# Performance work log

Hardware: AMD Instinct MI355X
Metric: run time of the kernel (lower is better)

Reference implementation:

```python
import jax, jax.numpy as jnp
import numpy as np
from functools import partial

B, S, H = 1, 2048, 1024
F, E, K = 2048, 8, 2


def setup_inputs() -> dict:
    key = jax.random.key(0)
    ks = jax.random.split(key, 7)
    x = jax.random.normal(ks[0], (B, S, H), dtype=jnp.float32)
    weights = jax.random.uniform(ks[1], (B * S, E), dtype=jnp.float32)
    top_weights = jax.random.uniform(ks[2], (B * S, K), dtype=jnp.float32)
    top_experts = jax.random.randint(ks[3], (B * S, K), 0, E).astype(jnp.int64)
    scale = 0.02  # keep activations in a sane range
    w1 = jax.random.normal(ks[4], (E, F, H), dtype=jnp.float32) * scale
    v1 = jax.random.normal(ks[5], (E, F, H), dtype=jnp.float32) * scale
    w2 = jax.random.normal(ks[6], (E, F, H), dtype=jnp.float32) * scale
    return {"x": x, "weights": weights, "top_weights": top_weights,
            "top_experts": top_experts, "w1": w1, "v1": v1, "w2": w2}


def _moe_forward(x, top_weights, top_experts, w1, v1, w2):
    b, s, h = x.shape
    xf = x.reshape(-1, h)  # [T, H]
    n_exp = w1.shape[0]
    # combine weight per (token, expert): sum over top-k slots routed to e
    onehot = jax.nn.one_hot(top_experts, n_exp, dtype=x.dtype)      # [T, K, E]
    cw = jnp.einsum('tk,tke->et', top_weights, onehot)              # [E, T]

    def body(acc, inputs):
        w1e, v1e, w2e, cwe = inputs  # [F,H], [F,H], [F,H], [T]
        gate = jax.nn.silu(xf @ w1e.T)       # [T, F]
        inter = gate * (xf @ v1e.T)          # GLU
        down = inter @ w2e                   # [T, H]
        return acc + cwe[:, None] * down, None

    out, _ = jax.lax.scan(body, jnp.zeros_like(xf), (w1, v1, w2, cw))
    return out.reshape(b, s, h)


def reference(x, weights, top_weights, top_experts, w1, v1, w2):
    # `weights` (full router probs) is accepted but unused, as in the original.
    return _moe_forward(x, top_weights, top_experts, w1, v1, w2)
```

## Files before the change

### kernel.cpp

```cpp
#include <hip/hip_runtime.h>
#include <hip/hip_bf16.h>


#define T_ 2048
#define H_ 1024
#define F_ 2048
#define E_ 8

#define SCAP 768
#define NSLOT (E_ * SCAP)
#define MAXT2 (NSLOT / 128)

typedef unsigned short u16;
typedef short s8v __attribute__((ext_vector_type(8)));
typedef float f4v __attribute__((ext_vector_type(4)));
typedef unsigned short u16x4 __attribute__((ext_vector_type(4)));

__device__ __forceinline__ u16 f2bf(float f) {
    union { float f; unsigned u; } v; v.f = f;
    unsigned r = v.u + 0x7FFF + ((v.u >> 16) & 1);
    return (u16)(r >> 16);
}
__device__ __forceinline__ unsigned pkbf(float a, float b) {
    __hip_bfloat162 h = __float22bfloat162_rn(make_float2(a, b));
    union { __hip_bfloat162 h; unsigned u; } c; c.h = h; return c.u;
}
__device__ __forceinline__ int4 cvt8(const float4 a, const float4 b) {
    int4 r; r.x = (int)pkbf(a.x, a.y); r.y = (int)pkbf(a.z, a.w);
    r.z = (int)pkbf(b.x, b.y); r.w = (int)pkbf(b.z, b.w); return r;
}
__device__ __forceinline__ void async16(void* lds, const void* g) {
    __builtin_amdgcn_global_load_lds(
        (const __attribute__((address_space(1))) unsigned*)g,
        (__attribute__((address_space(3))) unsigned*)lds, 16, 0, 0);
}

__global__ void router_kernel(const int* __restrict__ te, const float* __restrict__ tw,
                              int* __restrict__ slot_tok, float* __restrict__ slot_w,
                              int* __restrict__ tok_slot,
                              int* __restrict__ tile_e, int* __restrict__ tile_s,
                              int* __restrict__ ntiles) {
    __shared__ int cnt[E_];
    __shared__ int s_any;
    int tid = threadIdx.x;
    if (tid < E_) cnt[tid] = 0;
    if (tid == 0) s_any = 0;
    __syncthreads();
    int any = 0;
    for (int i = tid; i < 2 * T_; i += 256) if (i & 1) any |= te[i];
    if (any) atomicOr(&s_any, 1);
    __syncthreads();
    bool is32 = (s_any != 0);
    for (int t = tid; t < T_; t += 256) {
        int e0 = is32 ? te[2 * t]     : te[4 * t];
        int e1 = is32 ? te[2 * t + 1] : te[4 * t + 2];
        float w0 = tw[2 * t], w1 = tw[2 * t + 1];
        if (e0 == e1) {
            int p = atomicAdd(&cnt[e0], 1);
            int s = (p < SCAP) ? e0 * SCAP + p : -1;
            if (s >= 0) { slot_tok[s] = t; slot_w[s] = w0 + w1; }
            tok_slot[2 * t] = s; tok_slot[2 * t + 1] = -1;
        } else {
            int p = atomicAdd(&cnt[e0], 1);
            int s = (p < SCAP) ? e0 * SCAP + p : -1;
            if (s >= 0) { slot_tok[s] = t; slot_w[s] = w0; }
            tok_slot[2 * t] = s;
            p = atomicAdd(&cnt[e1], 1);
            s = (p < SCAP) ? e1 * SCAP + p : -1;
            if (s >= 0) { slot_tok[s] = t; slot_w[s] = w1; }
            tok_slot[2 * t + 1] = s;
        }
    }
    __syncthreads();
    for (int e = 0; e < E_; ++e) {
        int c = min(cnt[e], SCAP);
        int pc = min((c + 127) & ~127, SCAP);
        for (int p = c + tid; p < pc; p += 256) {
            slot_tok[e * SCAP + p] = -1; slot_w[e * SCAP + p] = 0.f;
        }
    }
    __syncthreads();
    if (tid == 0) {
        int nt = 0;
        for (int e = 0; e < E_; ++e) {
            int pc = min((min(cnt[e], SCAP) + 127) & ~127, SCAP);
            for (int s = 0; s < pc; s += 128) { tile_e[nt] = e; tile_s[nt] = e * SCAP + s; ++nt; }
        }
        *ntiles = nt;
    }
}

__global__ void cvtwv_kernel(const float* __restrict__ w1, const float* __restrict__ v1,
                             u16* __restrict__ w1b, u16* __restrict__ v1b) {
    const float* src = blockIdx.y ? v1 : w1;
    u16* dst = blockIdx.y ? v1b : w1b;
    int i = (blockIdx.x * 256 + threadIdx.x) * 4;
    float4 v = *(const float4*)(src + i);
    u16x4 o = { f2bf(v.x), f2bf(v.y), f2bf(v.z), f2bf(v.w) };
    *(u16x4*)(dst + i) = o;
}

__global__ void tcvt8_kernel(const float* __restrict__ src0, u16* __restrict__ dst0) {
    const float* src = src0 + (size_t)blockIdx.z * F_ * H_;
    u16* dst = dst0 + (size_t)blockIdx.z * H_ * F_;
    __shared__ __align__(16) u16 tile[64][72];
    int bc = blockIdx.x * 64, br = blockIdx.y * 64;
    int tx = threadIdx.x, ty = threadIdx.y;
    for (int r = ty; r < 64; r += 32) {
        const float* p = src + (size_t)(br + r) * H_ + bc + tx * 8;
        float4 v0 = *(const float4*)p;
        float4 v1 = *(const float4*)(p + 4);
        u16* q = &tile[r][tx * 8];
        q[0] = f2bf(v0.x); q[1] = f2bf(v0.y); q[2] = f2bf(v0.z); q[3] = f2bf(v0.w);
        q[4] = f2bf(v1.x); q[5] = f2bf(v1.y); q[6] = f2bf(v1.z); q[7] = f2bf(v1.w);
    }
    __syncthreads();
    for (int c = ty; c < 64; c += 32) {
        u16 tmp[8];
#pragma unroll
        for (int j = 0; j < 8; ++j) tmp[j] = tile[tx * 8 + j][c];
        *(int4*)&dst[(size_t)(bc + c) * F_ + br + tx * 8] = *(int4*)tmp;
    }
}

__global__ void gather_x_kernel(const float* __restrict__ x, const int* __restrict__ slot_tok,
                                const int* __restrict__ tile_s, const int* __restrict__ ntiles,
                                u16* __restrict__ xg) {
    if ((int)blockIdx.x >= *ntiles) return;
    int base = tile_s[blockIdx.x];
    int tid = threadIdx.x;
    __shared__ int stok[128];
    if (tid < 128) stok[tid] = slot_tok[base + tid];
    __syncthreads();
    for (int c = tid; c < 128 * 128; c += 256) {
        int r = c >> 7, co = (c & 127) * 8;
        int tok = stok[r];
        u16* dst = xg + ((size_t)(base + r) << 10) + co;
        if (tok < 0) { *(int4*)dst = make_int4(0, 0, 0, 0); }
        else {
            const float* p = x + ((size_t)tok << 10) + co;
            *(int4*)dst = cvt8(*(const float4*)p, *(const float4*)(p + 4));
        }
    }
}

__global__ __launch_bounds__(256, 4) void glu_async_kernel(
        const u16* __restrict__ xg, const u16* __restrict__ w1b,
        const u16* __restrict__ v1b, const int* __restrict__ tile_e,
        const int* __restrict__ tile_s, const int* __restrict__ ntiles,
        const float* __restrict__ slot_w, u16* __restrict__ inter) {
    int bt = blockIdx.y;
    if (bt >= *ntiles) return;
    int e = tile_e[bt], s0 = tile_s[bt];
    int f0 = blockIdx.x * 64;
    __shared__ __align__(16) u16 As[128 * 32];
    __shared__ __align__(16) u16 B1s[64 * 32];
    __shared__ __align__(16) u16 B2s[64 * 32];
    __shared__ float swv[128];
    int tid = threadIdx.x;
    int lane = tid & 63, wave = tid >> 6;
    int wm = wave >> 1, wn = wave & 1;
    int ml = lane & 15, q = lane >> 4;
    if (tid < 128) swv[tid] = slot_w[s0 + tid];

    int acol = (lane & 3) << 3;
    int row0 = (wave << 4) + (lane >> 2);
    int row1 = row0 + 64;
    const u16* gA0  = xg + ((size_t)(s0 + row0) << 10) + acol;
    const u16* gA1  = xg + ((size_t)(s0 + row1) << 10) + acol;
    const size_t wofs = (size_t)e * F_ * H_;
    const u16* gB1 = w1b + wofs + ((size_t)(f0 + row0) << 10) + acol;
    const u16* gB2 = v1b + wofs + ((size_t)(f0 + row0) << 10) + acol;
    u16* lA0 = As  + (row0 << 5) + acol;
    u16* lA1 = As  + (row1 << 5) + acol;
    u16* lB1 = B1s + (row0 << 5) + acol;
    u16* lB2 = B2s + (row0 << 5) + acol;

    f4v accg[4][2] = {};
    f4v accu[4][2] = {};

    for (int k0 = 0; k0 < H_; k0 += 32) {
        __syncthreads();
        async16(lA0, gA0 + k0);
        async16(lA1, gA1 + k0);
        async16(lB1, gB1 + k0);
        async16(lB2, gB2 + k0);
        __syncthreads();
        s8v a[4], b1[2], b2[2];
#pragma unroll
        for (int i = 0; i < 4; ++i)
            a[i]  = *(const s8v*)(As  + (wm * 64 + i * 16 + ml) * 32 + q * 8);
#pragma unroll
        for (int j = 0; j < 2; ++j) {
            b1[j] = *(const s8v*)(B1s + (wn * 32 + j * 16 + ml) * 32 + q * 8);
            b2[j] = *(const s8v*)(B2s + (wn * 32 + j * 16 + ml) * 32 + q * 8);
        }
#pragma unroll
        for (int i = 0; i < 4; ++i)
#pragma unroll
            for (int j = 0; j < 2; ++j) {
                accg[i][j] = __builtin_amdgcn_mfma_f32_16x16x32_bf16(a[i], b1[j], accg[i][j], 0, 0, 0);
                accu[i][j] = __builtin_amdgcn_mfma_f32_16x16x32_bf16(a[i], b2[j], accu[i][j], 0, 0, 0);
            }
    }
#pragma unroll
    for (int i = 0; i < 4; ++i)
#pragma unroll
        for (int r = 0; r < 4; ++r) {
            int lr = wm * 64 + i * 16 + q * 4 + r;
            float cv = swv[lr];
#pragma unroll
            for (int j = 0; j < 2; ++j) {
                float g = accg[i][j][r];
                float u = accu[i][j][r];
                float s = g / (1.f + __expf(-g));
                int f = f0 + wn * 32 + j * 16 + ml;
                inter[((size_t)(s0 + lr) << 11) + f] = f2bf(cv * s * u);
            }
        }
}

__global__ __launch_bounds__(256, 4) void down_async_kernel(
        const u16* __restrict__ inter, const u16* __restrict__ w2bT,
        const int* __restrict__ tile_e, const int* __restrict__ tile_s,
        const int* __restrict__ ntiles,
        float* __restrict__ dbufA, float* __restrict__ dbufB) {
    int bt = blockIdx.y;
    if (bt >= *ntiles) return;
    int e = tile_e[bt], s0 = tile_s[bt];
    int h0 = blockIdx.x * 64;
    int ks = blockIdx.z;
    int kbeg = ks * (F_ / 2);
    float* dbuf = ks ? dbufB : dbufA;
    __shared__ __align__(16) u16 As[128 * 32];
    __shared__ __align__(16) u16 Bs[64 * 32];
    int tid = threadIdx.x;
    int lane = tid & 63, wave = tid >> 6;
    int wm = wave >> 1, wn = wave & 1;
    int ml = lane & 15, q = lane >> 4;

    int acol = (lane & 3) << 3;
    int row0 = (wave << 4) + (lane >> 2);
    int row1 = row0 + 64;
    const u16* gA0 = inter + ((size_t)(s0 + row0) << 11) + kbeg + acol;
    const u16* gA1 = inter + ((size_t)(s0 + row1) << 11) + kbeg + acol;
    const u16* gB  = w2bT + (size_t)e * H_ * F_ + ((size_t)(h0 + row0) << 11) + kbeg + acol;
    u16* lA0 = As + (row0 << 5) + acol;
    u16* lA1 = As + (row1 << 5) + acol;
    u16* lB  = Bs + (row0 << 5) + acol;

    f4v acc[4][2] = {};
    for (int k0 = 0; k0 < F_ / 2; k0 += 32) {
        __syncthreads();
        async16(lA0, gA0 + k0);
        async16(lA1, gA1 + k0);
        async16(lB,  gB  + k0);
        __syncthreads();
        s8v a[4], b[2];
#pragma unroll
        for (int i = 0; i < 4; ++i)
            a[i] = *(const s8v*)(As + (wm * 64 + i * 16 + ml) * 32 + q * 8);
#pragma unroll
        for (int j = 0; j < 2; ++j)
            b[j] = *(const s8v*)(Bs + (wn * 32 + j * 16 + ml) * 32 + q * 8);
#pragma unroll
        for (int i = 0; i < 4; ++i)
#pragma unroll
            for (int j = 0; j < 2; ++j)
                acc[i][j] = __builtin_amdgcn_mfma_f32_16x16x32_bf16(a[i], b[j], acc[i][j], 0, 0, 0);
    }
#pragma unroll
    for (int i = 0; i < 4; ++i)
#pragma unroll
        for (int r = 0; r < 4; ++r) {
            int lr = wm * 64 + i * 16 + q * 4 + r;
            float* drow = dbuf + ((size_t)(s0 + lr) << 10);
#pragma unroll
            for (int j = 0; j < 2; ++j) {
                int h = h0 + wn * 32 + j * 16 + ml;
                drow[h] = acc[i][j][r];
            }
        }
}

__global__ void combine_kernel(const float* __restrict__ dbufA, const float* __restrict__ dbufB,
                               const int* __restrict__ tok_slot, float* __restrict__ out) {
    int t = blockIdx.x;
    int c = threadIdx.x * 4;
    int s0 = tok_slot[2 * t], s1 = tok_slot[2 * t + 1];
    float4 acc = make_float4(0.f, 0.f, 0.f, 0.f);
    if (s0 >= 0) {
        float4 a = *(const float4*)(dbufA + ((size_t)s0 << 10) + c);
        float4 b = *(const float4*)(dbufB + ((size_t)s0 << 10) + c);
        acc.x = a.x + b.x; acc.y = a.y + b.y; acc.z = a.z + b.z; acc.w = a.w + b.w;
    }
    if (s1 >= 0) {
        float4 a = *(const float4*)(dbufA + ((size_t)s1 << 10) + c);
        float4 b = *(const float4*)(dbufB + ((size_t)s1 << 10) + c);
        acc.x += a.x + b.x; acc.y += a.y + b.y; acc.z += a.z + b.z; acc.w += a.w + b.w;
    }
    *(float4*)(out + ((size_t)t << 10) + c) = acc;
}

#define SCAP3 1024
__global__ void router3_kernel(const int* __restrict__ te, const float* __restrict__ tw,
                               int* __restrict__ cnt_g, int* __restrict__ slot_tok,
                               float* __restrict__ slot_w) {
    __shared__ int cnt[E_];
    __shared__ int s_any;
    int tid = threadIdx.x;
    if (tid < E_) cnt[tid] = 0;
    if (tid == 0) s_any = 0;
    __syncthreads();
    int any = 0;
    for (int i = tid; i < 2 * T_; i += 256) if (i & 1) any |= te[i];
    if (any) atomicOr(&s_any, 1);
    __syncthreads();
    bool is32 = (s_any != 0);
    for (int t = tid; t < T_; t += 256) {
        int e0 = is32 ? te[2 * t]     : te[4 * t];
        int e1 = is32 ? te[2 * t + 1] : te[4 * t + 2];
        float w0 = tw[2 * t], w1 = tw[2 * t + 1];
        if (e0 == e1) {
            int p = atomicAdd(&cnt[e0], 1);
            if (p < SCAP3) { slot_tok[e0 * SCAP3 + p] = t; slot_w[e0 * SCAP3 + p] = w0 + w1; }
        } else {
            int p = atomicAdd(&cnt[e0], 1);
            if (p < SCAP3) { slot_tok[e0 * SCAP3 + p] = t; slot_w[e0 * SCAP3 + p] = w0; }
            p = atomicAdd(&cnt[e1], 1);
            if (p < SCAP3) { slot_tok[e1 * SCAP3 + p] = t; slot_w[e1 * SCAP3 + p] = w1; }
        }
    }
    __syncthreads();
    for (int e = 0; e < E_; ++e) {
        int c = min(cnt[e], SCAP3);
        int pc = min((c + 127) & ~127, SCAP3);
        for (int p = c + tid; p < pc; p += 256) {
            slot_tok[e * SCAP3 + p] = 0; slot_w[e * SCAP3 + p] = 0.f;
        }
    }
    if (tid < E_) cnt_g[tid] = min(cnt[tid], SCAP3);
}
__global__ void cvt_kernel(const float* __restrict__ src, u16* __restrict__ dst) {
    int i = (blockIdx.x * 256 + threadIdx.x) * 4;
    float4 v = *(const float4*)(src + i);
    u16x4 o = { f2bf(v.x), f2bf(v.y), f2bf(v.z), f2bf(v.w) };
    *(u16x4*)(dst + i) = o;
}
__global__ __launch_bounds__(256, 2) void glu3_kernel(
        const u16* __restrict__ xb, const float* __restrict__ w1,
        const float* __restrict__ v1, const int* __restrict__ cnt_g,
        const int* __restrict__ slot_tok, const float* __restrict__ slot_w,
        u16* __restrict__ inter) {
    int e = blockIdx.x >> 3, tt = blockIdx.x & 7;
    if (tt * 128 >= cnt_g[e]) return;
    __shared__ __align__(16) u16 As[128 * 32];
    __shared__ __align__(16) u16 B1s[128 * 32];
    __shared__ __align__(16) u16 B2s[128 * 32];
    __shared__ int stok[128];
    __shared__ float sw[128];
    int tid = threadIdx.x;
    if (tid < 128) {
        stok[tid] = slot_tok[e * SCAP3 + tt * 128 + tid];
        sw[tid]   = slot_w[e * SCAP3 + tt * 128 + tid];
    }
    __syncthreads();
    int lane = tid & 63, wave = tid >> 6;
    int wm = wave >> 1, wn = wave & 1;
    int f0 = blockIdx.y * 128;
    int ml = lane & 15, q = lane >> 4;
    int r0 = tid >> 2, r1 = 64 + (tid >> 2);
    int colo = (tid & 3) * 8;
    const size_t tokoff0 = (size_t)stok[r0] * H_ + colo;
    const size_t tokoff1 = (size_t)stok[r1] * H_ + colo;
    const float* gb1 = w1 + (size_t)e * F_ * H_ + (size_t)f0 * H_;
    const float* gb2 = v1 + (size_t)e * F_ * H_ + (size_t)f0 * H_;
    const size_t boff0 = (size_t)r0 * H_ + colo;
    const size_t boff1 = (size_t)r1 * H_ + colo;
    f4v accg[4][4] = {};
    f4v accu[4][4] = {};
    for (int k0 = 0; k0 < H_; k0 += 32) {
        __syncthreads();
        *(int4*)(As + tid * 8)         = *(const int4*)(xb + tokoff0 + k0);
        *(int4*)(As + (256 + tid) * 8) = *(const int4*)(xb + tokoff1 + k0);
        const float* p = gb1 + boff0 + k0;
        *(int4*)(B1s + tid * 8) = cvt8(*(const float4*)p, *(const float4*)(p + 4));
        p = gb1 + boff1 + k0;
        *(int4*)(B1s + (256 + tid) * 8) = cvt8(*(const float4*)p, *(const float4*)(p + 4));
        p = gb2 + boff0 + k0;
        *(int4*)(B2s + tid * 8) = cvt8(*(const float4*)p, *(const float4*)(p + 4));
        p = gb2 + boff1 + k0;
        *(int4*)(B2s + (256 + tid) * 8) = cvt8(*(const float4*)p, *(const float4*)(p + 4));
        __syncthreads();
        s8v a[4], b1[4], b2[4];
#pragma unroll
        for (int i = 0; i < 4; ++i) {
            a[i]  = *(const s8v*)(As  + (wm * 64 + i * 16 + ml) * 32 + q * 8);
            b1[i] = *(const s8v*)(B1s + (wn * 64 + i * 16 + ml) * 32 + q * 8);
            b2[i] = *(const s8v*)(B2s + (wn * 64 + i * 16 + ml) * 32 + q * 8);
        }
#pragma unroll
        for (int i = 0; i < 4; ++i)
#pragma unroll
            for (int j = 0; j < 4; ++j) {
                accg[i][j] = __builtin_amdgcn_mfma_f32_16x16x32_bf16(a[i], b1[j], accg[i][j], 0, 0, 0);
                accu[i][j] = __builtin_amdgcn_mfma_f32_16x16x32_bf16(a[i], b2[j], accu[i][j], 0, 0, 0);
            }
    }
#pragma unroll
    for (int i = 0; i < 4; ++i)
#pragma unroll
        for (int r = 0; r < 4; ++r) {
            int lr = wm * 64 + i * 16 + q * 4 + r;
            float cv = sw[lr];
#pragma unroll
            for (int j = 0; j < 4; ++j) {
                float g = accg[i][j][r];
                float u = accu[i][j][r];
                float s = g / (1.f + __expf(-g));
                int f = f0 + wn * 64 + j * 16 + ml;
                inter[(size_t)(e * SCAP3 + tt * 128 + lr) * F_ + f] = f2bf(cv * s * u);
            }
        }
}
__global__ __launch_bounds__(256) void down3_kernel(
        const u16* __restrict__ inter, const u16* __restrict__ w2bT,
        const int* __restrict__ cnt_g, const int* __restrict__ slot_tok,
        float* __restrict__ out) {
    int e = blockIdx.x >> 3, tt = blockIdx.x & 7;
    if (tt * 128 >= cnt_g[e]) return;
    __shared__ __align__(16) u16 As[128 * 32];
    __shared__ __align__(16) u16 Bs[128 * 32];
    __shared__ int stok[128];
    int tid = threadIdx.x;
    if (tid < 128) stok[tid] = slot_tok[e * SCAP3 + tt * 128 + tid];
    __syncthreads();
    int lane = tid & 63, wave = tid >> 6;
    int wm = wave >> 1, wn = wave & 1;
    int h0 = blockIdx.y * 128;
    int ml = lane & 15, q = lane >> 4;
    int kbeg = blockIdx.z * (F_ / 2), kend = kbeg + (F_ / 2);
    f4v acc[4][4] = {};
    const u16* ga = inter + (size_t)(e * SCAP3 + tt * 128) * F_;
    const u16* gb = w2bT + (size_t)e * H_ * F_ + (size_t)h0 * F_;
    for (int k0 = kbeg; k0 < kend; k0 += 32) {
        __syncthreads();
#pragma unroll
        for (int p = 0; p < 2; ++p) {
            int c = p * 256 + tid;
            int r = c >> 2, co = (c & 3) * 8;
            *(int4*)(As + c * 8) = *(const int4*)(ga + (size_t)r * F_ + k0 + co);
            *(int4*)(Bs + c * 8) = *(const int4*)(gb + (size_t)r * F_ + k0 + co);
        }
        __syncthreads();
        s8v a[4], b[4];
#pragma unroll
        for (int i = 0; i < 4; ++i) {
            a[i] = *(const s8v*)(As + (wm * 64 + i * 16 + ml) * 32 + q * 8);
            b[i] = *(const s8v*)(Bs + (wn * 64 + i * 16 + ml) * 32 + q * 8);
        }
#pragma unroll
        for (int i = 0; i < 4; ++i)
#pragma unroll
            for (int j = 0; j < 4; ++j)
                acc[i][j] = __builtin_amdgcn_mfma_f32_16x16x32_bf16(a[i], b[j], acc[i][j], 0, 0, 0);
    }
#pragma unroll
    for (int i = 0; i < 4; ++i)
#pragma unroll
        for (int r = 0; r < 4; ++r) {
            int lr = wm * 64 + i * 16 + q * 4 + r;
            size_t trow = (size_t)stok[lr] * H_;
#pragma unroll
            for (int j = 0; j < 4; ++j) {
                int h = h0 + wn * 64 + j * 16 + ml;
                atomicAdd(&out[trow + h], acc[i][j][r]);
            }
        }
}

extern "C" void kernel_launch(void* const* d_in, const int* in_sizes, int n_in,
                              void* d_out, int out_size, void* d_ws, size_t ws_size,
                              hipStream_t stream) {
    const float* x  = (const float*)d_in[0];
    const float* tw = (const float*)d_in[2];
    const int*   te = (const int*)d_in[3];
    const float* w1 = (const float*)d_in[4];
    const float* v1 = (const float*)d_in[5];
    const float* w2 = (const float*)d_in[6];
    float* out = (float*)d_out;
    char* ws = (char*)d_ws;

    if (ws_size >= ((size_t)135 << 20)) {
        int*   ntiles   = (int*)(ws);
        int*   tile_e   = (int*)(ws + 256);
        int*   tile_s   = (int*)(ws + 512);
        int*   tok_slot = (int*)(ws + (4 << 10));
        int*   slot_tok = (int*)(ws + (20 << 10));
        float* slot_w   = (float*)(ws + (44 << 10));
        u16*   xg       = (u16*)(ws + ((size_t)1 << 20));
        u16*   w1b      = (u16*)(ws + ((size_t)13 << 20));
        u16*   v1b      = (u16*)(ws + ((size_t)45 << 20));
        u16*   w2bT     = (u16*)(ws + ((size_t)77 << 20));
        u16*   inter    = (u16*)(ws + ((size_t)109 << 20));
        float* dbufA    = (float*)(ws + ((size_t)13 << 20));
        float* dbufB    = (float*)(ws + ((size_t)45 << 20));

        router_kernel<<<1, 256, 0, stream>>>(te, tw, slot_tok, slot_w, tok_slot,
                                             tile_e, tile_s, ntiles);
        cvtwv_kernel<<<dim3((E_ * F_ * H_) / 1024, 2), 256, 0, stream>>>(w1, v1, w1b, v1b);
        tcvt8_kernel<<<dim3(H_ / 64, F_ / 64, E_), dim3(8, 32), 0, stream>>>(w2, w2bT);
        gather_x_kernel<<<MAXT2, 256, 0, stream>>>(x, slot_tok, tile_s, ntiles, xg);
        glu_async_kernel<<<dim3(F_ / 64, MAXT2), 256, 0, stream>>>(
            xg, w1b, v1b, tile_e, tile_s, ntiles, slot_w, inter);
        down_async_kernel<<<dim3(H_ / 64, MAXT2, 2), 256, 0, stream>>>(
            inter, w2bT, tile_e, tile_s, ntiles, dbufA, dbufB);
        combine_kernel<<<T_, 256, 0, stream>>>(dbufA, dbufB, tok_slot, out);
    } else {
        int*   cnt_g    = (int*)(ws);
        int*   slot_tok = (int*)(ws + (4 << 10));
        float* slot_w   = (float*)(ws + (64 << 10));
        u16*   xb       = (u16*)(ws + ((size_t)1 << 20));
        u16*   w2bT     = (u16*)(ws + ((size_t)5 << 20));
        u16*   inter    = (u16*)(ws + ((size_t)37 << 20));

        hipMemsetAsync(out, 0, (size_t)T_ * H_ * sizeof(float), stream);
        router3_kernel<<<1, 256, 0, stream>>>(te, tw, cnt_g, slot_tok, slot_w);
        cvt_kernel<<<(T_ * H_) / 1024, 256, 0, stream>>>(x, xb);
        tcvt8_kernel<<<dim3(H_ / 64, F_ / 64, E_), dim3(8, 32), 0, stream>>>(w2, w2bT);
        glu3_kernel<<<dim3(E_ * 8, F_ / 128), 256, 0, stream>>>(
            xb, w1, v1, cnt_g, slot_tok, slot_w, inter);
        down3_kernel<<<dim3(E_ * 8, H_ / 128, 2), 256, 0, stream>>>(
            inter, w2bT, cnt_g, slot_tok, out);
    }
}
```

Before: 366.1 us.

## Double-buffer LDS with XOR swizzle in GEMMs, widen conversion and gather grids

Both GEMM kernels now double-buffer their LDS tiles. The next k-slice is prefetched with async loads while the current one feeds MFMA, and one barrier per iteration is removed. Column chunks are XOR-swizzled on store and read to cut LDS bank conflicts. The weight conversion kernel handles 8 elements per thread, and the gather kernel is split over 8 y-blocks for more parallelism. The doubled LDS footprint may limit occupancy, and relying on a single barrier assumes the async loads have completed before that barrier.

```diff
diff --git a/kernel.cpp b/kernel.cpp
--- a/kernel.cpp
+++ b/kernel.cpp
@@ -94,10 +94,10 @@
                              u16* __restrict__ w1b, u16* __restrict__ v1b) {
     const float* src = blockIdx.y ? v1 : w1;
     u16* dst = blockIdx.y ? v1b : w1b;
-    int i = (blockIdx.x * 256 + threadIdx.x) * 4;
-    float4 v = *(const float4*)(src + i);
-    u16x4 o = { f2bf(v.x), f2bf(v.y), f2bf(v.z), f2bf(v.w) };
-    *(u16x4*)(dst + i) = o;
+    int i = (blockIdx.x * 256 + threadIdx.x) * 8;
+    float4 a = *(const float4*)(src + i);
+    float4 b = *(const float4*)(src + i + 4);
+    *(int4*)(dst + i) = cvt8(a, b);
 }
 
 __global__ void tcvt8_kernel(const float* __restrict__ src0, u16* __restrict__ dst0) {
@@ -132,7 +132,8 @@
     __shared__ int stok[128];
     if (tid < 128) stok[tid] = slot_tok[base + tid];
     __syncthreads();
-    for (int c = tid; c < 128 * 128; c += 256) {
+    int c0 = blockIdx.y * 2048;
+    for (int c = c0 + tid; c < c0 + 2048; c += 256) {
         int r = c >> 7, co = (c & 127) * 8;
         int tok = stok[r];
         u16* dst = xg + ((size_t)(base + r) << 10) + co;
@@ -153,9 +154,9 @@
     if (bt >= *ntiles) return;
     int e = tile_e[bt], s0 = tile_s[bt];
     int f0 = blockIdx.x * 64;
-    __shared__ __align__(16) u16 As[128 * 32];
-    __shared__ __align__(16) u16 B1s[64 * 32];
-    __shared__ __align__(16) u16 B2s[64 * 32];
+    __shared__ __align__(16) u16 As[2][128 * 32];
+    __shared__ __align__(16) u16 B1s[2][64 * 32];
+    __shared__ __align__(16) u16 B2s[2][64 * 32];
     __shared__ float swv[128];
     int tid = threadIdx.x;
     int lane = tid & 63, wave = tid >> 6;
@@ -163,37 +164,44 @@
     int ml = lane & 15, q = lane >> 4;
     if (tid < 128) swv[tid] = slot_w[s0 + tid];
 
-    int acol = (lane & 3) << 3;
     int row0 = (wave << 4) + (lane >> 2);
     int row1 = row0 + 64;
-    const u16* gA0  = xg + ((size_t)(s0 + row0) << 10) + acol;
-    const u16* gA1  = xg + ((size_t)(s0 + row1) << 10) + acol;
+    int cs = ((lane & 3) ^ ((row0 >> 1) & 3)) << 3;
+    const u16* gA0  = xg + ((size_t)(s0 + row0) << 10) + cs;
+    const u16* gA1  = xg + ((size_t)(s0 + row1) << 10) + cs;
     const size_t wofs = (size_t)e * F_ * H_;
-    const u16* gB1 = w1b + wofs + ((size_t)(f0 + row0) << 10) + acol;
-    const u16* gB2 = v1b + wofs + ((size_t)(f0 + row0) << 10) + acol;
-    u16* lA0 = As  + (row0 << 5) + acol;
-    u16* lA1 = As  + (row1 << 5) + acol;
-    u16* lB1 = B1s + (row0 << 5) + acol;
-    u16* lB2 = B2s + (row0 << 5) + acol;
+    const u16* gB1 = w1b + wofs + ((size_t)(f0 + row0) << 10) + cs;
+    const u16* gB2 = v1b + wofs + ((size_t)(f0 + row0) << 10) + cs;
+    int l0 = (row0 << 5) + ((lane & 3) << 3);
+    int l1 = (row1 << 5) + ((lane & 3) << 3);
+    int xs = (q ^ ((lane >> 1) & 3)) << 3;
 
     f4v accg[4][2] = {};
     f4v accu[4][2] = {};
 
+    async16(&As[0][l0],  gA0);
+    async16(&As[0][l1],  gA1);
+    async16(&B1s[0][l0], gB1);
+    async16(&B2s[0][l0], gB2);
+
+    int cur = 0;
     for (int k0 = 0; k0 < H_; k0 += 32) {
         __syncthreads();
-        async16(lA0, gA0 + k0);
-        async16(lA1, gA1 + k0);
-        async16(lB1, gB1 + k0);
-        async16(lB2, gB2 + k0);
-        __syncthreads();
+        if (k0 + 32 < H_) {
+            int nx = cur ^ 1;
+            async16(&As[nx][l0],  gA0 + k0 + 32);
+            async16(&As[nx][l1],  gA1 + k0 + 32);
+            async16(&B1s[nx][l0], gB1 + k0 + 32);
+            async16(&B2s[nx][l0], gB2 + k0 + 32);
+        }
         s8v a[4], b1[2], b2[2];
 #pragma unroll
         for (int i = 0; i < 4; ++i)
-            a[i]  = *(const s8v*)(As  + (wm * 64 + i * 16 + ml) * 32 + q * 8);
+            a[i]  = *(const s8v*)(&As[cur][(wm * 64 + i * 16 + ml) * 32 + xs]);
 #pragma unroll
         for (int j = 0; j < 2; ++j) {
-            b1[j] = *(const s8v*)(B1s + (wn * 32 + j * 16 + ml) * 32 + q * 8);
-            b2[j] = *(const s8v*)(B2s + (wn * 32 + j * 16 + ml) * 32 + q * 8);
+            b1[j] = *(const s8v*)(&B1s[cur][(wn * 32 + j * 16 + ml) * 32 + xs]);
+            b2[j] = *(const s8v*)(&B2s[cur][(wn * 32 + j * 16 + ml) * 32 + xs]);
         }
 #pragma unroll
         for (int i = 0; i < 4; ++i)
@@ -202,6 +210,7 @@
                 accg[i][j] = __builtin_amdgcn_mfma_f32_16x16x32_bf16(a[i], b1[j], accg[i][j], 0, 0, 0);
                 accu[i][j] = __builtin_amdgcn_mfma_f32_16x16x32_bf16(a[i], b2[j], accu[i][j], 0, 0, 0);
             }
+        cur ^= 1;
     }
 #pragma unroll
     for (int i = 0; i < 4; ++i)
@@ -232,42 +241,51 @@
     int ks = blockIdx.z;
     int kbeg = ks * (F_ / 2);
     float* dbuf = ks ? dbufB : dbufA;
-    __shared__ __align__(16) u16 As[128 * 32];
-    __shared__ __align__(16) u16 Bs[64 * 32];
+    __shared__ __align__(16) u16 As[2][128 * 32];
+    __shared__ __align__(16) u16 Bs[2][64 * 32];
     int tid = threadIdx.x;
     int lane = tid & 63, wave = tid >> 6;
     int wm = wave >> 1, wn = wave & 1;
     int ml = lane & 15, q = lane >> 4;
 
-    int acol = (lane & 3) << 3;
     int row0 = (wave << 4) + (lane >> 2);
     int row1 = row0 + 64;
-    const u16* gA0 = inter + ((size_t)(s0 + row0) << 11) + kbeg + acol;
-    const u16* gA1 = inter + ((size_t)(s0 + row1) << 11) + kbeg + acol;
-    const u16* gB  = w2bT + (size_t)e * H_ * F_ + ((size_t)(h0 + row0) << 11) + kbeg + acol;
-    u16* lA0 = As + (row0 << 5) + acol;
-    u16* lA1 = As + (row1 << 5) + acol;
-    u16* lB  = Bs + (row0 << 5) + acol;
+    int cs = ((lane & 3) ^ ((row0 >> 1) & 3)) << 3;
+    const u16* gA0 = inter + ((size_t)(s0 + row0) << 11) + kbeg + cs;
+    const u16* gA1 = inter + ((size_t)(s0 + row1) << 11) + kbeg + cs;
+    const u16* gB  = w2bT + (size_t)e * H_ * F_ + ((size_t)(h0 + row0) << 11) + kbeg + cs;
+    int l0 = (row0 << 5) + ((lane & 3) << 3);
+    int l1 = (row1 << 5) + ((lane & 3) << 3);
+    int xs = (q ^ ((lane >> 1) & 3)) << 3;
 
     f4v acc[4][2] = {};
+
+    async16(&As[0][l0], gA0);
+    async16(&As[0][l1], gA1);
+    async16(&Bs[0][l0], gB);
+
+    int cur = 0;
     for (int k0 = 0; k0 < F_ / 2; k0 += 32) {
         __syncthreads();
-        async16(lA0, gA0 + k0);
-        async16(lA1, gA1 + k0);
-        async16(lB,  gB  + k0);
-        __syncthreads();
+        if (k0 + 32 < F_ / 2) {
+            int nx = cur ^ 1;
+            async16(&As[nx][l0], gA0 + k0 + 32);
+            async16(&As[nx][l1], gA1 + k0 + 32);
+            async16(&Bs[nx][l0], gB  + k0 + 32);
+        }
         s8v a[4], b[2];
 #pragma unroll
         for (int i = 0; i < 4; ++i)
-            a[i] = *(const s8v*)(As + (wm * 64 + i * 16 + ml) * 32 + q * 8);
+            a[i] = *(const s8v*)(&As[cur][(wm * 64 + i * 16 + ml) * 32 + xs]);
 #pragma unroll
         for (int j = 0; j < 2; ++j)
-            b[j] = *(const s8v*)(Bs + (wn * 32 + j * 16 + ml) * 32 + q * 8);
+            b[j] = *(const s8v*)(&Bs[cur][(wn * 32 + j * 16 + ml) * 32 + xs]);
 #pragma unroll
         for (int i = 0; i < 4; ++i)
 #pragma unroll
             for (int j = 0; j < 2; ++j)
                 acc[i][j] = __builtin_amdgcn_mfma_f32_16x16x32_bf16(a[i], b[j], acc[i][j], 0, 0, 0);
+        cur ^= 1;
     }
 #pragma unroll
     for (int i = 0; i < 4; ++i)
@@ -508,9 +526,9 @@
 
         router_kernel<<<1, 256, 0, stream>>>(te, tw, slot_tok, slot_w, tok_slot,
                                              tile_e, tile_s, ntiles);
-        cvtwv_kernel<<<dim3((E_ * F_ * H_) / 1024, 2), 256, 0, stream>>>(w1, v1, w1b, v1b);
+        cvtwv_kernel<<<dim3((E_ * F_ * H_) / 2048, 2), 256, 0, stream>>>(w1, v1, w1b, v1b);
         tcvt8_kernel<<<dim3(H_ / 64, F_ / 64, E_), dim3(8, 32), 0, stream>>>(w2, w2bT);
-        gather_x_kernel<<<MAXT2, 256, 0, stream>>>(x, slot_tok, tile_s, ntiles, xg);
+        gather_x_kernel<<<dim3(MAXT2, 8), 256, 0, stream>>>(x, slot_tok, tile_s, ntiles, xg);
         glu_async_kernel<<<dim3(F_ / 64, MAXT2), 256, 0, stream>>>(
             xg, w1b, v1b, tile_e, tile_s, ntiles, slot_w, inter);
         down_async_kernel<<<dim3(H_ / 64, MAXT2, 2), 256, 0, stream>>>(
```

New measurement: 338.5 us. 1.08x faster.
